# Performance work log

Measured on AMD Instinct MI355X. Metric: run time of the kernel, lower is better.

Reference implementation:

```python
import jax, jax.numpy as jnp
import numpy as np

X_MIN, X_MAX = -40.0, 40.0
Y_MIN, Y_MAX = -40.0, 40.0
Z_MIN, Z_MAX = -3.0, 1.0
SX, SY = 0.16, 0.16
NX, NY = 500, 500
SENT = NX * NY            # sentinel linear index for invalid points
MAX_PILLARS = 12000
MAX_PTS = 100
OUT_CH = 64
EPS = 1e-5


def _bn(x, g, b, m, v):
    return (x - m) * (g * jax.lax.rsqrt(v + EPS)) + b


def _scene(pts, W1, g1, b1, rm1, rv1, W2, g2, b2, rm2, rv2):
    # pts: (N,4) = [x,y,z,intensity]
    x, y, z = pts[:, 0], pts[:, 1], pts[:, 2]
    valid = ((x >= X_MIN) & (x < X_MAX) & (y >= Y_MIN) & (y < Y_MAX)
             & (z >= Z_MIN) & (z < Z_MAX))
    xi = jnp.floor((x - X_MIN) / SX).astype(jnp.int32)
    yi = jnp.floor((y - Y_MIN) / SY).astype(jnp.int32)
    # linear pillar id; lexicographic (x,y) order == ascending xi*NY+yi,
    # matching torch.unique(dim=0) sorted output
    lin = jnp.where(valid, xi * NY + yi, SENT)
    # primary key: pillar id asc; secondary: z descending (torch argsort desc)
    order = jnp.lexsort((-z, lin))
    lin_s = lin[order]
    pts_s = pts[order]
    n = lin_s.shape[0]
    is_new = jnp.concatenate([jnp.ones((1,), bool), lin_s[1:] != lin_s[:-1]])
    rank = jnp.cumsum(is_new) - 1                     # pillar rank per point
    idx = jnp.arange(n)
    pos = idx - jax.lax.cummax(jnp.where(is_new, idx, 0))  # slot within pillar
    valid_s = lin_s < SENT
    keep = valid_s & (rank < MAX_PILLARS) & (pos < MAX_PTS)
    tp = jnp.where(keep, rank, MAX_PILLARS)
    tq = jnp.where(keep, pos, 0)
    # scatter points into (P, M, 4) buffer; dropped points go to dummy row P
    buf = (jnp.zeros((MAX_PILLARS + 1, MAX_PTS, 4), pts.dtype)
           .at[tp, tq].set(jnp.where(keep[:, None], pts_s, 0.0)))[:MAX_PILLARS]

    # unique pillar coords (first occurrence per rank)
    new_keep = is_new & valid_s & (rank < MAX_PILLARS)
    tu = jnp.where(new_keep, rank, MAX_PILLARS)
    lin_u = (jnp.zeros((MAX_PILLARS + 1,), jnp.int32)
             .at[tu].set(lin_s.astype(jnp.int32)))[:MAX_PILLARS]
    num = jnp.sum(new_keep)
    pvalid = jnp.arange(MAX_PILLARS) < num
    px = jnp.where(pvalid, lin_u // NY, 0)
    py = jnp.where(pvalid, lin_u % NY, 0)

    xc = px.astype(pts.dtype) * SX + X_MIN + SX / 2   # (P,)
    yc = py.astype(pts.dtype) * SY + Y_MIN + SY / 2
    xc_b = jnp.broadcast_to(xc[:, None], (MAX_PILLARS, MAX_PTS))
    yc_b = jnp.broadcast_to(yc[:, None], (MAX_PILLARS, MAX_PTS))
    # channels: [x, y, z, i, x_c, y_c, x-x_c, y-y_c]; note padded point rows
    # get offsets -x_c/-y_c exactly like the torch code (offset after padding)
    feats = jnp.stack([buf[..., 0], buf[..., 1], buf[..., 2], buf[..., 3],
                       xc_b, yc_b,
                       buf[..., 0] - xc[:, None], buf[..., 1] - yc[:, None]],
                      axis=-1)                         # (P, M, 8)

    h = jax.nn.relu(_bn(feats @ W1.T, g1, b1, rm1, rv1))   # (P, M, 64)
    h = jax.nn.relu(_bn(h @ W2.T, g2, b2, rm2, rv2))       # (P, M, 64)
    pooled = jnp.max(h, axis=1)                            # max over points
    feats_out = jnp.where(pvalid[:, None], pooled, 0.0)    # zero-pad pillars
    coords = jnp.stack([jnp.zeros_like(px), px, py], axis=1)  # (P, 3)
    return feats_out, coords


def setup_inputs() -> dict:
    key = jax.random.key(0)
    ks = jax.random.split(key, 15)
    B, N = 2, 150000
    xy = jax.random.uniform(ks[0], (B, N, 2), minval=-42.0, maxval=42.0)
    zz = jax.random.uniform(ks[1], (B, N, 1), minval=-3.5, maxval=1.5)
    it = jax.random.uniform(ks[2], (B, N, 1))
    points = jnp.concatenate([xy, zz, it], axis=-1)
    W1 = jax.random.normal(ks[3], (OUT_CH, 8), jnp.float32) * 0.1
    W2 = jax.random.normal(ks[4], (OUT_CH, OUT_CH), jnp.float32) * 0.1
    g1 = jax.random.uniform(ks[5], (OUT_CH,), minval=0.5, maxval=1.5)
    b1 = jax.random.normal(ks[6], (OUT_CH,)) * 0.1
    rm1 = jax.random.normal(ks[7], (OUT_CH,)) * 0.1
    rv1 = jax.random.uniform(ks[8], (OUT_CH,), minval=0.5, maxval=1.5)
    g2 = jax.random.uniform(ks[9], (OUT_CH,), minval=0.5, maxval=1.5)
    b2 = jax.random.normal(ks[10], (OUT_CH,)) * 0.1
    rm2 = jax.random.normal(ks[11], (OUT_CH,)) * 0.1
    rv2 = jax.random.uniform(ks[12], (OUT_CH,), minval=0.5, maxval=1.5)
    return {"points": points, "W1": W1, "g1": g1, "b1": b1, "rm1": rm1,
            "rv1": rv1, "W2": W2, "g2": g2, "b2": b2, "rm2": rm2, "rv2": rv2}


def reference(points, W1, g1, b1, rm1, rv1, W2, g2, b2, rm2, rv2):
    fn = lambda p: _scene(p, W1, g1, b1, rm1, rv1, W2, g2, b2, rm2, rv2)
    pillar_features, coords = jax.vmap(fn)(points)
    return pillar_features, coords
```

## Files before the change

### kernel.cpp

```cpp
#include <hip/hip_runtime.h>
#include <float.h>

#define NXY      250000
#define NYG      500
#define MAXP     12000
#define CAP      16
#define NPTS     150000
#define BATCH    2
#define NV16     15625
#define NB       62
#define NWAVE_MLP 4096

__device__ __forceinline__ int cell_of(float x, float y, float z, bool& ok) {
    bool valid = (x >= -40.0f) & (x < 40.0f) & (y >= -40.0f) & (y < 40.0f)
               & (z >= -3.0f)  & (z < 1.0f);
    int xi = (int)floorf((x - (-40.0f)) / 0.16f);
    int yi = (int)floorf((y - (-40.0f)) / 0.16f);
    int lin = xi * NYG + yi;
    ok = valid && ((unsigned)lin < (unsigned)NXY);
    return lin;
}

__global__ void k_occ(const float4* __restrict__ pts, unsigned char* __restrict__ occ) {
    int g = blockIdx.x * blockDim.x + threadIdx.x;
    if (g >= BATCH * NPTS) return;
    int b = g / NPTS;
    float4 p = pts[g];
    bool ok; int lin = cell_of(p.x, p.y, p.z, ok);
    if (ok) occ[b * NXY + lin] = 1;
}

__global__ void k_blocksum(const int4* __restrict__ occ4, int* __restrict__ bs) {
    int b = blockIdx.y, blk = blockIdx.x, tid = threadIdx.x;
    int idx = blk * 256 + tid;
    int s = 0;
    if (idx < NV16) {
        int4 v = occ4[b * NV16 + idx];
        s = __popc(v.x) + __popc(v.y) + __popc(v.z) + __popc(v.w);
    }
#pragma unroll
    for (int off = 32; off >= 1; off >>= 1) s += __shfl_down(s, off, 64);
    __shared__ int wt[4];
    int lane = tid & 63, wv = tid >> 6;
    if (lane == 0) wt[wv] = s;
    __syncthreads();
    if (tid == 0) bs[b * NB + blk] = wt[0] + wt[1] + wt[2] + wt[3];
}

__global__ void k_scan(const int* __restrict__ bs, int* __restrict__ bo, int* __restrict__ num) {
    int b = blockIdx.x, tid = threadIdx.x;
    int v = (tid < NB) ? bs[b * NB + tid] : 0;
    int incl = v;
#pragma unroll
    for (int off = 1; off < 64; off <<= 1) {
        int n = __shfl_up(incl, off, 64);
        if (tid >= off) incl += n;
    }
    if (tid < NB) bo[b * NB + tid] = incl - v;
    if (tid == 63) num[b] = incl < MAXP ? incl : MAXP;
}

__global__ void k_rank(const int4* __restrict__ occ4, const int* __restrict__ bo,
                       ushort* __restrict__ cellRank, int* __restrict__ pillarLin) {
    int b = blockIdx.y, blk = blockIdx.x, tid = threadIdx.x;
    int idx = blk * 256 + tid;
    int4 v = make_int4(0, 0, 0, 0);
    if (idx < NV16) v = occ4[b * NV16 + idx];
    int s = __popc(v.x) + __popc(v.y) + __popc(v.z) + __popc(v.w);
    int lane = tid & 63, wv = tid >> 6;
    int incl = s;
#pragma unroll
    for (int off = 1; off < 64; off <<= 1) {
        int n = __shfl_up(incl, off, 64);
        if (lane >= off) incl += n;
    }
    __shared__ int wt[4];
    if (lane == 63) wt[wv] = incl;
    __syncthreads();
    int woff = 0;
    for (int w = 0; w < wv; w++) woff += wt[w];
    if (idx >= NV16) return;
    int run = bo[b * NB + blk] + woff + (incl - s);
    int cell = idx * 16;
    unsigned char ob[16];
    *(int4*)ob = v;
    union { ushort u[16]; int4 q[2]; } r;
#pragma unroll
    for (int i = 0; i < 16; i++) {
        ushort t = 0xFFFFu;
        if (ob[i]) {
            if (run < MAXP) { t = (ushort)run; pillarLin[b * MAXP + run] = cell + i; }
            run++;
        }
        r.u[i] = t;
    }
    int4* dst = (int4*)(cellRank + b * NXY + cell);
    dst[0] = r.q[0];
    dst[1] = r.q[1];
}

__global__ void k_scatter(const float4* __restrict__ pts, const ushort* __restrict__ cellRank,
                          int* __restrict__ pcnt, float4* __restrict__ pbuf) {
    int g = blockIdx.x * blockDim.x + threadIdx.x;
    if (g >= BATCH * NPTS) return;
    int b = g / NPTS;
    float4 p = pts[g];
    bool ok; int lin = cell_of(p.x, p.y, p.z, ok);
    if (!ok) return;
    ushort r = cellRank[b * NXY + lin];
    if (r == 0xFFFFu) return;
    int q = b * MAXP + (int)r;
    int slot = atomicAdd(&pcnt[q], 1);
    if (slot < CAP) pbuf[q * CAP + slot] = p;
}

__global__ __launch_bounds__(256, 2) void k_mlp(
    const float4* __restrict__ pbuf, const int* __restrict__ num,
    const int* __restrict__ pillarLin, const int* __restrict__ pcnt,
    const float* __restrict__ W1, const float* __restrict__ g1, const float* __restrict__ b1,
    const float* __restrict__ rm1, const float* __restrict__ rv1,
    const float* __restrict__ W2, const float* __restrict__ g2, const float* __restrict__ b2,
    const float* __restrict__ rm2, const float* __restrict__ rv2,
    float* __restrict__ out) {
    int lane = threadIdx.x & 63, wv = threadIdx.x >> 6;
    int wg = blockIdx.x * 4 + wv;
    __shared__ float h1s[4][64];
    int c = lane;

    float4 w1a = *(const float4*)(W1 + c * 8);
    float4 w1b = *(const float4*)(W1 + c * 8 + 4);
    float s1 = g1[c] / sqrtf(rv1[c] + 1e-5f);
    float mb1 = rm1[c], ab1 = b1[c];
    float4 w2[16];
#pragma unroll
    for (int i = 0; i < 16; i++) w2[i] = *(const float4*)(W2 + c * 64 + i * 4);
    float s2 = g2[c] / sqrtf(rv2[c] + 1e-5f);
    float mb2 = rm2[c], ab2 = b2[c];

    float wxx = w1a.x + w1b.z, wyy = w1a.y + w1b.w;
    float wzz = w1a.z, wii = w1a.w;
    float cwx = w1b.x - w1b.z, cwy = w1b.y - w1b.w;
    float* outC = out + (size_t)BATCH * MAXP * 64;

    for (int q = wg; q < BATCH * MAXP; q += NWAVE_MLP) {
        int b = q / MAXP, p = q - b * MAXP;
        float* of = out + (size_t)q * 64;
        if (p >= num[b]) {
            of[lane] = 0.0f;
            if (lane < 3) outC[q * 3 + lane] = 0.0f;
            continue;
        }
        int lin = pillarLin[q];
        int pxg = lin / NYG, pyg = lin - pxg * NYG;
        float xc = (float)pxg * 0.16f + (-40.0f) + 0.08f;
        float yc = (float)pyg * 0.16f + (-40.0f) + 0.08f;
        int cnt = pcnt[q];
        int m = cnt < CAP ? cnt : CAP;
        float4 mypt = pbuf[q * CAP + (lane & 15)];
        float dbase = xc * cwx + yc * cwy;
        float pooled = -FLT_MAX;
        for (int j = 0; j <= m; j++) {
            float d;
            if (j < m) {
                float x  = __shfl(mypt.x, j, 64);
                float y  = __shfl(mypt.y, j, 64);
                float z  = __shfl(mypt.z, j, 64);
                float it = __shfl(mypt.w, j, 64);
                d = dbase + x * wxx + y * wyy + z * wzz + it * wii;
            } else {
                if (cnt >= 100) break;
                d = dbase;
            }
            float h1 = fmaxf((d - mb1) * s1 + ab1, 0.0f);
            h1s[wv][lane] = h1;
            float a0 = 0.f, a1 = 0.f, a2 = 0.f, a3 = 0.f;
#pragma unroll
            for (int kk = 0; kk < 4; kk++) {
                float4 h0 = *(float4*)&h1s[wv][(kk * 4 + 0) * 4];
                float4 h1v = *(float4*)&h1s[wv][(kk * 4 + 1) * 4];
                float4 h2v = *(float4*)&h1s[wv][(kk * 4 + 2) * 4];
                float4 h3v = *(float4*)&h1s[wv][(kk * 4 + 3) * 4];
                float4 wA = w2[kk * 4 + 0], wB = w2[kk * 4 + 1];
                float4 wC = w2[kk * 4 + 2], wD = w2[kk * 4 + 3];
                a0 += h0.x * wA.x + h0.y * wA.y + h0.z * wA.z + h0.w * wA.w;
                a1 += h1v.x * wB.x + h1v.y * wB.y + h1v.z * wB.z + h1v.w * wB.w;
                a2 += h2v.x * wC.x + h2v.y * wC.y + h2v.z * wC.z + h2v.w * wC.w;
                a3 += h3v.x * wD.x + h3v.y * wD.y + h3v.z * wD.z + h3v.w * wD.w;
            }
            float acc = (a0 + a1) + (a2 + a3);
            float h2 = fmaxf((acc - mb2) * s2 + ab2, 0.0f);
            pooled = fmaxf(pooled, h2);
        }
        of[lane] = pooled;
        if (lane < 3)
            outC[q * 3 + lane] = (lane == 0) ? 0.0f : ((lane == 1) ? (float)pxg : (float)pyg);
    }
}

extern "C" void kernel_launch(void* const* d_in, const int* in_sizes, int n_in,
                              void* d_out, int out_size, void* d_ws, size_t ws_size,
                              hipStream_t stream) {
    const float4* pts = (const float4*)d_in[0];
    const float* W1  = (const float*)d_in[1];
    const float* g1  = (const float*)d_in[2];
    const float* b1  = (const float*)d_in[3];
    const float* rm1 = (const float*)d_in[4];
    const float* rv1 = (const float*)d_in[5];
    const float* W2  = (const float*)d_in[6];
    const float* g2  = (const float*)d_in[7];
    const float* b2  = (const float*)d_in[8];
    const float* rm2 = (const float*)d_in[9];
    const float* rv2 = (const float*)d_in[10];

    char* w = (char*)d_ws;
    unsigned char* occ = (unsigned char*)(w + 0);
    int*    pcnt       = (int*)(w + 500000);
    ushort* cellRank   = (ushort*)(w + 596000);
    int*    bs         = (int*)(w + 1596000);
    int*    bo         = (int*)(w + 1596496);
    int*    num        = (int*)(w + 1596992);
    int*    pillarLin  = (int*)(w + 1597008);
    float4* pbuf       = (float4*)(w + 1693008);

    hipMemsetAsync(w, 0, 596000, stream);

    int ptBlocks = (BATCH * NPTS + 255) / 256;
    k_occ<<<ptBlocks, 256, 0, stream>>>(pts, occ);
    dim3 gb(NB, BATCH);
    k_blocksum<<<gb, 256, 0, stream>>>((const int4*)occ, bs);
    k_scan<<<BATCH, 64, 0, stream>>>(bs, bo, num);
    k_rank<<<gb, 256, 0, stream>>>((const int4*)occ, bo, cellRank, pillarLin);
    k_scatter<<<ptBlocks, 256, 0, stream>>>(pts, cellRank, pcnt, pbuf);
    k_mlp<<<NWAVE_MLP / 4, 256, 0, stream>>>(pbuf, num, pillarLin, pcnt,
                                             W1, g1, b1, rm1, rv1, W2, g2, b2, rm2, rv2,
                                             (float*)d_out);
}
```

Before: 120.4 us.

## Fuse block-sum and scan kernels, use readlane MLP, prefetch next pillar

Merges the block-sum and scan kernels into a single per-batch 1024-thread kernel that also zeroes the pillar counters, which shrinks the memset and removes one launch. The MLP kernel replaces the LDS round trip for the hidden layer with readlane broadcasts against W2 held in registers. It also prefetches the next pillar's data before computing the current one and raises launch bounds to 4 blocks. The single-block scan serializes 16 loads per thread, and holding 64 weight registers under the higher occupancy target risks spills.

```diff
diff --git a/kernel.cpp b/kernel.cpp
--- a/kernel.cpp
+++ b/kernel.cpp
@@ -7,9 +7,15 @@
 #define CAP      16
 #define NPTS     150000
 #define BATCH    2
+#define TOTP     (BATCH * MAXP)
 #define NV16     15625
 #define NB       62
+#define BO_STRIDE 64
 #define NWAVE_MLP 4096
+
+__device__ __forceinline__ float rl(float v, int l) {
+    return __int_as_float(__builtin_amdgcn_readlane(__float_as_int(v), l));
+}
 
 __device__ __forceinline__ int cell_of(float x, float y, float z, bool& ok) {
     bool valid = (x >= -40.0f) & (x < 40.0f) & (y >= -40.0f) & (y < 40.0f)
@@ -30,34 +36,36 @@
     if (ok) occ[b * NXY + lin] = 1;
 }
 
-__global__ void k_blocksum(const int4* __restrict__ occ4, int* __restrict__ bs) {
-    int b = blockIdx.y, blk = blockIdx.x, tid = threadIdx.x;
-    int idx = blk * 256 + tid;
+__global__ __launch_bounds__(1024) void k_sumscan(const int4* __restrict__ occ4,
+                                                  int* __restrict__ bo, int* __restrict__ num,
+                                                  int* __restrict__ pcnt) {
+    int b = blockIdx.x, tid = threadIdx.x;
+    for (int i = tid; i < MAXP; i += 1024) pcnt[b * MAXP + i] = 0;
+    int base = tid * 16;
     int s = 0;
-    if (idx < NV16) {
-        int4 v = occ4[b * NV16 + idx];
-        s = __popc(v.x) + __popc(v.y) + __popc(v.z) + __popc(v.w);
-    }
-#pragma unroll
-    for (int off = 32; off >= 1; off >>= 1) s += __shfl_down(s, off, 64);
-    __shared__ int wt[4];
+#pragma unroll
+    for (int i = 0; i < 16; i++) {
+        int idx = base + i;
+        if (idx < NV16) {
+            int4 v = occ4[b * NV16 + idx];
+            s += __popc(v.x) + __popc(v.y) + __popc(v.z) + __popc(v.w);
+        }
+    }
     int lane = tid & 63, wv = tid >> 6;
-    if (lane == 0) wt[wv] = s;
-    __syncthreads();
-    if (tid == 0) bs[b * NB + blk] = wt[0] + wt[1] + wt[2] + wt[3];
-}
-
-__global__ void k_scan(const int* __restrict__ bs, int* __restrict__ bo, int* __restrict__ num) {
-    int b = blockIdx.x, tid = threadIdx.x;
-    int v = (tid < NB) ? bs[b * NB + tid] : 0;
-    int incl = v;
+    int incl = s;
 #pragma unroll
     for (int off = 1; off < 64; off <<= 1) {
         int n = __shfl_up(incl, off, 64);
-        if (tid >= off) incl += n;
-    }
-    if (tid < NB) bo[b * NB + tid] = incl - v;
-    if (tid == 63) num[b] = incl < MAXP ? incl : MAXP;
+        if (lane >= off) incl += n;
+    }
+    __shared__ int wt[16];
+    if (lane == 63) wt[wv] = incl;
+    __syncthreads();
+    int woff = 0;
+    for (int w = 0; w < wv; w++) woff += wt[w];
+    int ex = woff + incl - s;
+    if ((tid & 15) == 0) bo[b * BO_STRIDE + (tid >> 4)] = ex;
+    if (tid == 1023) { int total = woff + incl; num[b] = total < MAXP ? total : MAXP; }
 }
 
 __global__ void k_rank(const int4* __restrict__ occ4, const int* __restrict__ bo,
@@ -80,7 +88,7 @@
     int woff = 0;
     for (int w = 0; w < wv; w++) woff += wt[w];
     if (idx >= NV16) return;
-    int run = bo[b * NB + blk] + woff + (incl - s);
+    int run = bo[b * BO_STRIDE + blk] + woff + (incl - s);
     int cell = idx * 16;
     unsigned char ob[16];
     *(int4*)ob = v;
@@ -114,7 +122,7 @@
     if (slot < CAP) pbuf[q * CAP + slot] = p;
 }
 
-__global__ __launch_bounds__(256, 2) void k_mlp(
+__global__ __launch_bounds__(256, 4) void k_mlp(
     const float4* __restrict__ pbuf, const int* __restrict__ num,
     const int* __restrict__ pillarLin, const int* __restrict__ pcnt,
     const float* __restrict__ W1, const float* __restrict__ g1, const float* __restrict__ b1,
@@ -124,76 +132,85 @@
     float* __restrict__ out) {
     int lane = threadIdx.x & 63, wv = threadIdx.x >> 6;
     int wg = blockIdx.x * 4 + wv;
-    __shared__ float h1s[4][64];
     int c = lane;
 
     float4 w1a = *(const float4*)(W1 + c * 8);
     float4 w1b = *(const float4*)(W1 + c * 8 + 4);
     float s1 = g1[c] / sqrtf(rv1[c] + 1e-5f);
     float mb1 = rm1[c], ab1 = b1[c];
-    float4 w2[16];
-#pragma unroll
-    for (int i = 0; i < 16; i++) w2[i] = *(const float4*)(W2 + c * 64 + i * 4);
+    float w2r[64];
+#pragma unroll
+    for (int i = 0; i < 16; i++) *(float4*)&w2r[i * 4] = *(const float4*)(W2 + c * 64 + i * 4);
     float s2 = g2[c] / sqrtf(rv2[c] + 1e-5f);
     float mb2 = rm2[c], ab2 = b2[c];
 
     float wxx = w1a.x + w1b.z, wyy = w1a.y + w1b.w;
     float wzz = w1a.z, wii = w1a.w;
     float cwx = w1b.x - w1b.z, cwy = w1b.y - w1b.w;
-    float* outC = out + (size_t)BATCH * MAXP * 64;
-
-    for (int q = wg; q < BATCH * MAXP; q += NWAVE_MLP) {
-        int b = q / MAXP, p = q - b * MAXP;
+    int n0 = num[0], n1 = num[1];
+    float* outC = out + (size_t)TOTP * 64;
+
+    int q = wg;
+    int lin = pillarLin[q];
+    int cnt = pcnt[q];
+    float4 mypt = pbuf[(size_t)q * CAP + (lane & 15)];
+    while (true) {
+        int qn = q + NWAVE_MLP;
+        bool more = qn < TOTP;
+        int linN = 0, cntN = 0;
+        float4 ptN = make_float4(0.f, 0.f, 0.f, 0.f);
+        if (more) {
+            linN = pillarLin[qn];
+            cntN = pcnt[qn];
+            ptN  = pbuf[(size_t)qn * CAP + (lane & 15)];
+        }
+
+        int b = q >= MAXP ? 1 : 0;
+        int p = q - b * MAXP;
+        int nb = b ? n1 : n0;
         float* of = out + (size_t)q * 64;
-        if (p >= num[b]) {
+        if (p >= nb) {
             of[lane] = 0.0f;
             if (lane < 3) outC[q * 3 + lane] = 0.0f;
-            continue;
-        }
-        int lin = pillarLin[q];
-        int pxg = lin / NYG, pyg = lin - pxg * NYG;
-        float xc = (float)pxg * 0.16f + (-40.0f) + 0.08f;
-        float yc = (float)pyg * 0.16f + (-40.0f) + 0.08f;
-        int cnt = pcnt[q];
-        int m = cnt < CAP ? cnt : CAP;
-        float4 mypt = pbuf[q * CAP + (lane & 15)];
-        float dbase = xc * cwx + yc * cwy;
-        float pooled = -FLT_MAX;
-        for (int j = 0; j <= m; j++) {
-            float d;
-            if (j < m) {
-                float x  = __shfl(mypt.x, j, 64);
-                float y  = __shfl(mypt.y, j, 64);
-                float z  = __shfl(mypt.z, j, 64);
-                float it = __shfl(mypt.w, j, 64);
-                d = dbase + x * wxx + y * wyy + z * wzz + it * wii;
-            } else {
-                if (cnt >= 100) break;
-                d = dbase;
+        } else {
+            int pxg = lin / NYG, pyg = lin - pxg * NYG;
+            float xc = (float)pxg * 0.16f + (-40.0f) + 0.08f;
+            float yc = (float)pyg * 0.16f + (-40.0f) + 0.08f;
+            float dbase = xc * cwx + yc * cwy;
+            int m = cnt < CAP ? cnt : CAP;
+            float pooled = -FLT_MAX;
+            for (int j = 0; j <= m; j++) {
+                float d;
+                if (j < m) {
+                    float x  = rl(mypt.x, j);
+                    float y  = rl(mypt.y, j);
+                    float z  = rl(mypt.z, j);
+                    float it = rl(mypt.w, j);
+                    d = dbase + x * wxx + y * wyy + z * wzz + it * wii;
+                } else {
+                    if (cnt >= 100) break;
+                    d = dbase;
+                }
+                float h1 = fmaxf((d - mb1) * s1 + ab1, 0.0f);
+                float a0 = 0.f, a1 = 0.f, a2 = 0.f, a3 = 0.f;
+#pragma unroll
+                for (int k = 0; k < 16; k++) {
+                    a0 = fmaf(rl(h1, k),      w2r[k],      a0);
+                    a1 = fmaf(rl(h1, k + 16), w2r[16 + k], a1);
+                    a2 = fmaf(rl(h1, k + 32), w2r[32 + k], a2);
+                    a3 = fmaf(rl(h1, k + 48), w2r[48 + k], a3);
+                }
+                float acc = (a0 + a1) + (a2 + a3);
+                float h2 = fmaxf((acc - mb2) * s2 + ab2, 0.0f);
+                pooled = fmaxf(pooled, h2);
             }
-            float h1 = fmaxf((d - mb1) * s1 + ab1, 0.0f);
-            h1s[wv][lane] = h1;
-            float a0 = 0.f, a1 = 0.f, a2 = 0.f, a3 = 0.f;
-#pragma unroll
-            for (int kk = 0; kk < 4; kk++) {
-                float4 h0 = *(float4*)&h1s[wv][(kk * 4 + 0) * 4];
-                float4 h1v = *(float4*)&h1s[wv][(kk * 4 + 1) * 4];
-                float4 h2v = *(float4*)&h1s[wv][(kk * 4 + 2) * 4];
-                float4 h3v = *(float4*)&h1s[wv][(kk * 4 + 3) * 4];
-                float4 wA = w2[kk * 4 + 0], wB = w2[kk * 4 + 1];
-                float4 wC = w2[kk * 4 + 2], wD = w2[kk * 4 + 3];
-                a0 += h0.x * wA.x + h0.y * wA.y + h0.z * wA.z + h0.w * wA.w;
-                a1 += h1v.x * wB.x + h1v.y * wB.y + h1v.z * wB.z + h1v.w * wB.w;
-                a2 += h2v.x * wC.x + h2v.y * wC.y + h2v.z * wC.z + h2v.w * wC.w;
-                a3 += h3v.x * wD.x + h3v.y * wD.y + h3v.z * wD.z + h3v.w * wD.w;
-            }
-            float acc = (a0 + a1) + (a2 + a3);
-            float h2 = fmaxf((acc - mb2) * s2 + ab2, 0.0f);
-            pooled = fmaxf(pooled, h2);
-        }
-        of[lane] = pooled;
-        if (lane < 3)
-            outC[q * 3 + lane] = (lane == 0) ? 0.0f : ((lane == 1) ? (float)pxg : (float)pyg);
+            of[lane] = pooled;
+            if (lane < 3)
+                outC[q * 3 + lane] = (lane == 0) ? 0.0f : ((lane == 1) ? (float)pxg : (float)pyg);
+        }
+
+        if (!more) break;
+        q = qn; lin = linN; cnt = cntN; mypt = ptN;
     }
 }
 
@@ -216,19 +233,17 @@
     unsigned char* occ = (unsigned char*)(w + 0);
     int*    pcnt       = (int*)(w + 500000);
     ushort* cellRank   = (ushort*)(w + 596000);
-    int*    bs         = (int*)(w + 1596000);
-    int*    bo         = (int*)(w + 1596496);
-    int*    num        = (int*)(w + 1596992);
-    int*    pillarLin  = (int*)(w + 1597008);
-    float4* pbuf       = (float4*)(w + 1693008);
-
-    hipMemsetAsync(w, 0, 596000, stream);
+    int*    bo         = (int*)(w + 1596000);
+    int*    num        = (int*)(w + 1596512);
+    int*    pillarLin  = (int*)(w + 1596528);
+    float4* pbuf       = (float4*)(w + 1692528);
+
+    hipMemsetAsync(w, 0, 500000, stream);
 
     int ptBlocks = (BATCH * NPTS + 255) / 256;
     k_occ<<<ptBlocks, 256, 0, stream>>>(pts, occ);
+    k_sumscan<<<BATCH, 1024, 0, stream>>>((const int4*)occ, bo, num, pcnt);
     dim3 gb(NB, BATCH);
-    k_blocksum<<<gb, 256, 0, stream>>>((const int4*)occ, bs);
-    k_scan<<<BATCH, 64, 0, stream>>>(bs, bo, num);
     k_rank<<<gb, 256, 0, stream>>>((const int4*)occ, bo, cellRank, pillarLin);
     k_scatter<<<ptBlocks, 256, 0, stream>>>(pts, cellRank, pcnt, pbuf);
     k_mlp<<<NWAVE_MLP / 4, 256, 0, stream>>>(pbuf, num, pillarLin, pcnt,
```

New measurement: 126.6 us. 1.05x slower.
